# Kernel tuning notes

Hardware: AMD Instinct MI355X
Metric: run time of the kernel (lower is better)

Reference implementation:

```python
import jax, jax.numpy as jnp
import numpy as np

MARGIN = 1.0
EPS = 1e-6  # torch F.pairwise_distance default eps, added elementwise to (x - y)
NEG_INF = -1e30
POS_INF = 1e30


def _pairwise_dist_matrix(e):
    # D[i,j] = || e_i - e_j + EPS ||_2, expanded so we never materialize [B,B,D]:
    # ||d + eps||^2 = ||d||^2 + 2*eps*sum(d) + Dfeat*eps^2,  d = e_i - e_j
    sq = jnp.sum(e * e, axis=1)          # [B]
    s = jnp.sum(e, axis=1)               # [B]
    d2 = (sq[:, None] + sq[None, :] - 2.0 * (e @ e.T)
          + 2.0 * EPS * (s[:, None] - s[None, :])
          + e.shape[1] * (EPS * EPS))
    return jnp.sqrt(jnp.maximum(d2, 0.0))  # [B,B]


def _pdist(x, y):
    # F.pairwise_distance(p=2): ||x - y + eps||
    return jnp.sqrt(jnp.sum(jnp.square(x - y + EPS), axis=-1))


def setup_inputs() -> dict:
    B, D = 4096, 128
    key = jax.random.key(0)
    k1, k2, k3, k4 = jax.random.split(key, 4)
    embedding = jax.random.normal(k1, (B, D), dtype=jnp.float32)
    # label space == batch, each label appears exactly once in the batch
    target_idx = jax.random.permutation(k2, B).astype(jnp.int32)
    positive_idxs = jax.random.bernoulli(k3, 0.02, (B, B))  # [B, L] label-space mask
    negative_idxs = jax.random.bernoulli(k4, 0.5, (B, B))
    return {"embedding": embedding, "target_idx": target_idx,
            "positive_idxs": positive_idxs, "negative_idxs": negative_idxs}


def reference(embedding, target_idx, positive_idxs, negative_idxs):
    # Mining happens under no_grad in the original module.
    dm = jax.lax.stop_gradient(_pairwise_dist_matrix(embedding))  # [B,B]
    # batch j is a positive/negative candidate for anchor i iff its label is flagged
    pos_mask = positive_idxs[:, target_idx]  # [B,B] bool
    neg_mask = negative_idxs[:, target_idx]
    pos_idx = jnp.argmax(jnp.where(pos_mask, dm, NEG_INF), axis=1)  # hardest positive
    neg_idx = jnp.argmin(jnp.where(neg_mask, dm, POS_INF), axis=1)  # hardest negative
    valid = jnp.any(pos_mask, axis=1) & jnp.any(neg_mask, axis=1)
    a = embedding
    p = embedding[pos_idx]
    n = embedding[neg_idx]
    ap = _pdist(a, p)
    an = _pdist(a, n)
    pn = _pdist(p, n)
    loss = jax.nn.relu(ap - jnp.minimum(an, pn) + MARGIN)
    w = valid.astype(loss.dtype)
    return jnp.sum(loss * w) / jnp.maximum(jnp.sum(w), 1.0)
```

## Files before the change

### kernel.cpp

```cpp
#include <hip/hip_runtime.h>
#include <stdint.h>

#define BN 4096
#define DD 128
#define EPSF 1e-6f
#define MARGINF 1.0f
#define TM 128
#define TN 128
#define KC 64

typedef unsigned long long ull;
typedef short short8 __attribute__((ext_vector_type(8)));
typedef float f32x4 __attribute__((ext_vector_type(4)));

__device__ __forceinline__ unsigned int ord_f32(float f) {
    unsigned int u = __float_as_uint(f);
    return (u & 0x80000000u) ? ~u : (u | 0x80000000u);
}
__device__ __forceinline__ unsigned short bf16_rne(float x) {
    unsigned int u = __float_as_uint(x);
    return (unsigned short)((u + 0x7FFFu + ((u >> 16) & 1u)) >> 16);
}

__global__ void k_prep(const float* __restrict__ e, const int* __restrict__ tidx,
                       float* __restrict__ sq, float* __restrict__ s,
                       int* __restrict__ inv, ull* __restrict__ pk, ull* __restrict__ nk,
                       unsigned int* __restrict__ ehi, unsigned int* __restrict__ elo) {
    int w = threadIdx.x >> 6, lane = threadIdx.x & 63;
    int row = blockIdx.x * 4 + w;
    float2 v = ((const float2*)(e + (size_t)row * DD))[lane];
    unsigned short hx = bf16_rne(v.x), hy = bf16_rne(v.y);
    float rx = v.x - __uint_as_float((unsigned int)hx << 16);
    float ry = v.y - __uint_as_float((unsigned int)hy << 16);
    unsigned short lx = bf16_rne(rx), ly = bf16_rne(ry);
    ehi[row * 64 + lane] = (unsigned int)hx | ((unsigned int)hy << 16);
    elo[row * 64 + lane] = (unsigned int)lx | ((unsigned int)ly << 16);
    float ss = v.x + v.y;
    float qq = v.x * v.x + v.y * v.y;
    #pragma unroll
    for (int off = 32; off > 0; off >>= 1) {
        ss += __shfl_down(ss, off);
        qq += __shfl_down(qq, off);
    }
    if (lane == 0) {
        sq[row] = qq; s[row] = ss;
        inv[tidx[row]] = row;
        pk[row] = 0ULL; nk[row] = ~0ULL;
    }
}

__global__ void k_bits(const int* __restrict__ pos, const int* __restrict__ neg,
                       ull* __restrict__ pb, ull* __restrict__ nb) {
    int row = blockIdx.x;
    int w = threadIdx.x >> 6, lane = threadIdx.x & 63;
    const int* pr = pos + (size_t)row * BN;
    const int* nr = neg + (size_t)row * BN;
    #pragma unroll 4
    for (int g = 0; g < 16; g++) {
        int col = g * 256 + w * 64 + lane;
        ull b = __ballot(pr[col] != 0);
        if (lane == 0) pb[row * 64 + g * 4 + w] = b;
        b = __ballot(nr[col] != 0);
        if (lane == 0) nb[row * 64 + g * 4 + w] = b;
    }
}

__global__ __launch_bounds__(256, 2)
void k_select(const unsigned short* __restrict__ ehi, const unsigned short* __restrict__ elo,
              const float* __restrict__ sq, const float* __restrict__ s,
              const int* __restrict__ inv,
              const ull* __restrict__ pbits, const ull* __restrict__ nbits,
              ull* __restrict__ pkey, ull* __restrict__ nkey) {
    __shared__ __align__(16) char smem[73728];
    __shared__ int   jvs[TN];
    __shared__ float ri[TM], rj[TN];
    __shared__ ull   pbl[256], nbl[256];

    unsigned short* Ah = (unsigned short*)smem;
    unsigned short* Alo = Ah + 9216;
    unsigned short* Bh = Ah + 18432;
    unsigned short* Blo = Ah + 27648;
    float* Dl = (float*)smem;

    const int tid = threadIdx.x;
    const int i0 = blockIdx.x * TM;
    const int c0 = blockIdx.y * TN;

    if (tid < TN) {
        int j = inv[c0 + tid];
        jvs[tid] = j;
        rj[tid] = sq[j] - 2.0f * EPSF * s[j];
        ri[tid] = sq[i0 + tid] + 2.0f * EPSF * s[i0 + tid];
    }
    {
        int irow = tid >> 1, half = tid & 1;
        size_t bidx = (size_t)(i0 + irow) * 64 + (c0 >> 6) + half;
        pbl[tid] = pbits[bidx];
        nbl[tid] = nbits[bidx];
    }

    const int lane = tid & 63, w = tid >> 6;
    const int lrow = lane & 15, quad = lane >> 4;

    f32x4 acc[2][8];
    #pragma unroll
    for (int rt = 0; rt < 2; rt++)
        #pragma unroll
        for (int ct = 0; ct < 8; ct++)
            acc[rt][ct] = (f32x4){0.f, 0.f, 0.f, 0.f};

    for (int kc = 0; kc < DD / KC; kc++) {
        __syncthreads();
        {
            int rr0 = tid >> 3, seg = tid & 7;
            #pragma unroll
            for (int p = 0; p < 4; p++) {
                int rr = p * 32 + rr0;
                int ar = i0 + rr;
                int jr = jvs[rr];
                int4 va = ((const int4*)(ehi + (size_t)ar * DD))[kc * 8 + seg];
                int4 vb = ((const int4*)(elo + (size_t)ar * DD))[kc * 8 + seg];
                *(int4*)(Ah + rr * 72 + seg * 8) = va;
                *(int4*)(Alo + rr * 72 + seg * 8) = vb;
                va = ((const int4*)(ehi + (size_t)jr * DD))[kc * 8 + seg];
                vb = ((const int4*)(elo + (size_t)jr * DD))[kc * 8 + seg];
                *(int4*)(Bh + rr * 72 + seg * 8) = va;
                *(int4*)(Blo + rr * 72 + seg * 8) = vb;
            }
        }
        __syncthreads();

        #pragma unroll
        for (int ks = 0; ks < 2; ks++) {
            const int kof = ks * 32 + quad * 8;
            short8 ahi[2], alo2[2];
            #pragma unroll
            for (int rt = 0; rt < 2; rt++) {
                const unsigned short* ap = Ah + (w * 32 + rt * 16 + lrow) * 72 + kof;
                const unsigned short* lp = Alo + (w * 32 + rt * 16 + lrow) * 72 + kof;
                ahi[rt] = *(const short8*)ap;
                alo2[rt] = *(const short8*)lp;
            }
            #pragma unroll
            for (int ct = 0; ct < 8; ct++) {
                const unsigned short* bp = Bh + (ct * 16 + lrow) * 72 + kof;
                const unsigned short* blp = Blo + (ct * 16 + lrow) * 72 + kof;
                short8 bhi = *(const short8*)bp;
                short8 blo = *(const short8*)blp;
                #pragma unroll
                for (int rt = 0; rt < 2; rt++) {
                    acc[rt][ct] = __builtin_amdgcn_mfma_f32_16x16x32_bf16(ahi[rt], bhi, acc[rt][ct], 0, 0, 0);
                    acc[rt][ct] = __builtin_amdgcn_mfma_f32_16x16x32_bf16(ahi[rt], blo, acc[rt][ct], 0, 0, 0);
                    acc[rt][ct] = __builtin_amdgcn_mfma_f32_16x16x32_bf16(alo2[rt], bhi, acc[rt][ct], 0, 0, 0);
                }
            }
        }
    }

    __syncthreads();
    #pragma unroll
    for (int rt = 0; rt < 2; rt++)
        #pragma unroll
        for (int ct = 0; ct < 8; ct++) {
            int rbase = w * 32 + rt * 16 + quad * 4;
            int col = ct * 16 + lrow;
            #pragma unroll
            for (int t = 0; t < 4; t++)
                Dl[(rbase + t) * 132 + col] = acc[rt][ct][t];
        }
    __syncthreads();

    const int tx = tid & 15, ty = tid >> 4;
    float bpv[8], bnv[8]; int bpi[8], bni[8];
    #pragma unroll
    for (int r = 0; r < 8; r++) {
        bpv[r] = -3.4e38f; bnv[r] = 3.4e38f;
        bpi[r] = 0x7FFFFFFF; bni[r] = 0x7FFFFFFF;
    }
    const int shift = (tx & 7) * 8;
    #pragma unroll
    for (int r = 0; r < 8; r++) {
        int irow = ty * 8 + r;
        float4 d0 = *(const float4*)&Dl[irow * 132 + tx * 8];
        float4 d1 = *(const float4*)&Dl[irow * 132 + tx * 8 + 4];
        float dot[8] = {d0.x, d0.y, d0.z, d0.w, d1.x, d1.y, d1.z, d1.w};
        unsigned int pb = (unsigned int)((pbl[irow * 2 + (tx >> 3)] >> shift) & 0xFFu);
        unsigned int nb = (unsigned int)((nbl[irow * 2 + (tx >> 3)] >> shift) & 0xFFu);
        float riv = ri[irow];
        #pragma unroll
        for (int c = 0; c < 8; c++) {
            int jl = tx * 8 + c;
            float d2 = riv + rj[jl] - 2.0f * dot[c] + (float)DD * EPSF * EPSF;
            int j = jvs[jl];
            if ((pb >> c) & 1u) {
                if (d2 > bpv[r] || (d2 == bpv[r] && j < bpi[r])) { bpv[r] = d2; bpi[r] = j; }
            }
            if ((nb >> c) & 1u) {
                if (d2 < bnv[r] || (d2 == bnv[r] && j < bni[r])) { bnv[r] = d2; bni[r] = j; }
            }
        }
    }

    __syncthreads();
    float* spv = (float*)smem;
    int*   spi = (int*)(spv + 2048);
    float* snv = (float*)(spi + 2048);
    int*   sni = (int*)(snv + 2048);
    #pragma unroll
    for (int r = 0; r < 8; r++) {
        int row = ty * 8 + r;
        spv[row * 16 + tx] = bpv[r]; spi[row * 16 + tx] = bpi[r];
        snv[row * 16 + tx] = bnv[r]; sni[row * 16 + tx] = bni[r];
    }
    __syncthreads();
    if (tid < TM) {
        float bv = -3.4e38f, nv = 3.4e38f;
        int bi = 0x7FFFFFFF, ni = 0x7FFFFFFF;
        for (int t = 0; t < 16; t++) {
            float v = spv[tid * 16 + t]; int ix = spi[tid * 16 + t];
            if (ix != 0x7FFFFFFF && (v > bv || (v == bv && ix < bi))) { bv = v; bi = ix; }
            v = snv[tid * 16 + t]; ix = sni[tid * 16 + t];
            if (ix != 0x7FFFFFFF && (v < nv || (v == nv && ix < ni))) { nv = v; ni = ix; }
        }
        if (bi != 0x7FFFFFFF) {
            ull key = ((ull)ord_f32(bv) << 32) | (ull)(0xFFFFFFFFu - (unsigned)bi);
            atomicMax(&pkey[i0 + tid], key);
        }
        if (ni != 0x7FFFFFFF) {
            ull key = ((ull)ord_f32(nv) << 32) | (ull)(unsigned)ni;
            atomicMin(&nkey[i0 + tid], key);
        }
    }
}

__global__ void k_loss(const float* __restrict__ e,
                       const ull* __restrict__ pkey, const ull* __restrict__ nkey,
                       float* __restrict__ partials) {
    int w = threadIdx.x >> 6, lane = threadIdx.x & 63;
    int row = blockIdx.x * 4 + w;
    ull pk = pkey[row], nk = nkey[row];
    float loss = 0.0f, wt = 0.0f;
    if (pk != 0ULL && nk != ~0ULL) {
        int pi = (int)(0xFFFFFFFFu - (unsigned)(pk & 0xFFFFFFFFu));
        int ni = (int)(unsigned)(nk & 0xFFFFFFFFu);
        float2 av = ((const float2*)(e + (size_t)row * DD))[lane];
        float2 pv = ((const float2*)(e + (size_t)pi * DD))[lane];
        float2 nv = ((const float2*)(e + (size_t)ni * DD))[lane];
        float dx, dy;
        dx = av.x - pv.x + EPSF; dy = av.y - pv.y + EPSF;
        float ap2 = dx * dx + dy * dy;
        dx = av.x - nv.x + EPSF; dy = av.y - nv.y + EPSF;
        float an2 = dx * dx + dy * dy;
        dx = pv.x - nv.x + EPSF; dy = pv.y - nv.y + EPSF;
        float pn2 = dx * dx + dy * dy;
        #pragma unroll
        for (int off = 32; off > 0; off >>= 1) {
            ap2 += __shfl_down(ap2, off);
            an2 += __shfl_down(an2, off);
            pn2 += __shfl_down(pn2, off);
        }
        if (lane == 0) {
            float ap = sqrtf(ap2), an = sqrtf(an2), pn = sqrtf(pn2);
            loss = fmaxf(ap - fminf(an, pn) + MARGINF, 0.0f);
            wt = 1.0f;
        }
    }
    __shared__ float sl[4], sw[4];
    if (lane == 0) { sl[w] = loss; sw[w] = wt; }
    __syncthreads();
    if (threadIdx.x == 0) {
        partials[blockIdx.x * 2 + 0] = sl[0] + sl[1] + sl[2] + sl[3];
        partials[blockIdx.x * 2 + 1] = sw[0] + sw[1] + sw[2] + sw[3];
    }
}

__global__ void k_final(const float* __restrict__ partials, float* __restrict__ out) {
    int tid = threadIdx.x;
    float L = 0.0f, W = 0.0f;
    for (int i = 0; i < 4; i++) {
        int idx = tid + i * 256;
        L += partials[idx * 2];
        W += partials[idx * 2 + 1];
    }
    #pragma unroll
    for (int off = 32; off > 0; off >>= 1) {
        L += __shfl_down(L, off);
        W += __shfl_down(W, off);
    }
    __shared__ float sl[4], sw[4];
    int w = tid >> 6, lane = tid & 63;
    if (lane == 0) { sl[w] = L; sw[w] = W; }
    __syncthreads();
    if (tid == 0) {
        float Lt = sl[0] + sl[1] + sl[2] + sl[3];
        float Wt = sw[0] + sw[1] + sw[2] + sw[3];
        out[0] = Lt / fmaxf(Wt, 1.0f);
    }
}

extern "C" void kernel_launch(void* const* d_in, const int* in_sizes, int n_in,
                              void* d_out, int out_size, void* d_ws, size_t ws_size,
                              hipStream_t stream) {
    const float* e    = (const float*)d_in[0];
    const int*   tidx = (const int*)d_in[1];
    const int*   pos  = (const int*)d_in[2];
    const int*   neg  = (const int*)d_in[3];
    float* out = (float*)d_out;

    ull* pkey  = (ull*)d_ws;
    ull* nkey  = pkey + BN;
    ull* pbits = nkey + BN;
    ull* nbits = pbits + BN * 64;
    float* sq  = (float*)(nbits + BN * 64);
    float* s   = sq + BN;
    int* inv   = (int*)(s + BN);
    float* partials = (float*)(inv + BN);
    unsigned int* ehi = (unsigned int*)(partials + 2048);
    unsigned int* elo = ehi + BN * 64;

    k_prep<<<BN / 4, 256, 0, stream>>>(e, tidx, sq, s, inv, pkey, nkey, ehi, elo);
    k_bits<<<BN, 256, 0, stream>>>(pos, neg, pbits, nbits);
    dim3 grid(BN / TM, BN / TN);
    k_select<<<grid, 256, 0, stream>>>((const unsigned short*)ehi, (const unsigned short*)elo,
                                       sq, s, inv, pbits, nbits, pkey, nkey);
    k_loss<<<BN / 4, 256, 0, stream>>>(e, pkey, nkey, partials);
    k_final<<<1, 256, 0, stream>>>(partials, out);
}
```

Baseline: 209.2 us.

## Load MFMA operands directly from global, keep selection in registers, vectorize mask packing

The selection kernel stops staging the hi/lo bf16 operand tiles in shared memory. Each wave now loads its A and gathered B fragments straight from global memory into registers. Hardest positive and negative selection runs directly on the accumulator registers rather than going through a shared-memory distance tile, which removes several barriers and LDS round trips and allows three blocks per CU. The mask-packing kernel reads sixteen ints per thread with int4 loads and writes packed 16-bit words instead of using ballots. The cost is that the four waves each fetch the same B fragments, relying on L1/L2 to absorb the duplicated loads.

```diff
diff --git a/kernel.cpp b/kernel.cpp
--- a/kernel.cpp
+++ b/kernel.cpp
@@ -7,9 +7,9 @@
 #define MARGINF 1.0f
 #define TM 128
 #define TN 128
-#define KC 64
 
 typedef unsigned long long ull;
+typedef unsigned short ushort;
 typedef short short8 __attribute__((ext_vector_type(8)));
 typedef float f32x4 __attribute__((ext_vector_type(4)));
 
@@ -17,9 +17,9 @@
     unsigned int u = __float_as_uint(f);
     return (u & 0x80000000u) ? ~u : (u | 0x80000000u);
 }
-__device__ __forceinline__ unsigned short bf16_rne(float x) {
+__device__ __forceinline__ ushort bf16_rne(float x) {
     unsigned int u = __float_as_uint(x);
-    return (unsigned short)((u + 0x7FFFu + ((u >> 16) & 1u)) >> 16);
+    return (ushort)((u + 0x7FFFu + ((u >> 16) & 1u)) >> 16);
 }
 
 __global__ void k_prep(const float* __restrict__ e, const int* __restrict__ tidx,
@@ -29,10 +29,10 @@
     int w = threadIdx.x >> 6, lane = threadIdx.x & 63;
     int row = blockIdx.x * 4 + w;
     float2 v = ((const float2*)(e + (size_t)row * DD))[lane];
-    unsigned short hx = bf16_rne(v.x), hy = bf16_rne(v.y);
+    ushort hx = bf16_rne(v.x), hy = bf16_rne(v.y);
     float rx = v.x - __uint_as_float((unsigned int)hx << 16);
     float ry = v.y - __uint_as_float((unsigned int)hy << 16);
-    unsigned short lx = bf16_rne(rx), ly = bf16_rne(ry);
+    ushort lx = bf16_rne(rx), ly = bf16_rne(ry);
     ehi[row * 64 + lane] = (unsigned int)hx | ((unsigned int)hy << 16);
     elo[row * 64 + lane] = (unsigned int)lx | ((unsigned int)ly << 16);
     float ss = v.x + v.y;
@@ -50,57 +50,65 @@
 }
 
 __global__ void k_bits(const int* __restrict__ pos, const int* __restrict__ neg,
-                       ull* __restrict__ pb, ull* __restrict__ nb) {
-    int row = blockIdx.x;
-    int w = threadIdx.x >> 6, lane = threadIdx.x & 63;
-    const int* pr = pos + (size_t)row * BN;
-    const int* nr = neg + (size_t)row * BN;
-    #pragma unroll 4
-    for (int g = 0; g < 16; g++) {
-        int col = g * 256 + w * 64 + lane;
-        ull b = __ballot(pr[col] != 0);
-        if (lane == 0) pb[row * 64 + g * 4 + w] = b;
-        b = __ballot(nr[col] != 0);
-        if (lane == 0) nb[row * 64 + g * 4 + w] = b;
-    }
-}
-
-__global__ __launch_bounds__(256, 2)
-void k_select(const unsigned short* __restrict__ ehi, const unsigned short* __restrict__ elo,
+                       ushort* __restrict__ pb, ushort* __restrict__ nb) {
+    const int row = blockIdx.x, t = threadIdx.x;
+    const int4* pr = (const int4*)(pos + (size_t)row * BN) + t * 4;
+    const int4* nr = (const int4*)(neg + (size_t)row * BN) + t * 4;
+    int4 p0 = pr[0], p1 = pr[1], p2 = pr[2], p3 = pr[3];
+    int4 n0 = nr[0], n1 = nr[1], n2 = nr[2], n3 = nr[3];
+    unsigned int m = 0;
+    m |= (p0.x != 0) << 0;  m |= (p0.y != 0) << 1;  m |= (p0.z != 0) << 2;  m |= (p0.w != 0) << 3;
+    m |= (p1.x != 0) << 4;  m |= (p1.y != 0) << 5;  m |= (p1.z != 0) << 6;  m |= (p1.w != 0) << 7;
+    m |= (p2.x != 0) << 8;  m |= (p2.y != 0) << 9;  m |= (p2.z != 0) << 10; m |= (p2.w != 0) << 11;
+    m |= (p3.x != 0) << 12; m |= (p3.y != 0) << 13; m |= (p3.z != 0) << 14; m |= (p3.w != 0) << 15;
+    pb[(size_t)row * 256 + t] = (ushort)m;
+    m = 0;
+    m |= (n0.x != 0) << 0;  m |= (n0.y != 0) << 1;  m |= (n0.z != 0) << 2;  m |= (n0.w != 0) << 3;
+    m |= (n1.x != 0) << 4;  m |= (n1.y != 0) << 5;  m |= (n1.z != 0) << 6;  m |= (n1.w != 0) << 7;
+    m |= (n2.x != 0) << 8;  m |= (n2.y != 0) << 9;  m |= (n2.z != 0) << 10; m |= (n2.w != 0) << 11;
+    m |= (n3.x != 0) << 12; m |= (n3.y != 0) << 13; m |= (n3.z != 0) << 14; m |= (n3.w != 0) << 15;
+    nb[(size_t)row * 256 + t] = (ushort)m;
+}
+
+__global__ __launch_bounds__(256, 3)
+void k_select(const ushort* __restrict__ ehi, const ushort* __restrict__ elo,
               const float* __restrict__ sq, const float* __restrict__ s,
               const int* __restrict__ inv,
               const ull* __restrict__ pbits, const ull* __restrict__ nbits,
               ull* __restrict__ pkey, ull* __restrict__ nkey) {
-    __shared__ __align__(16) char smem[73728];
-    __shared__ int   jvs[TN];
-    __shared__ float ri[TM], rj[TN];
-    __shared__ ull   pbl[256], nbl[256];
-
-    unsigned short* Ah = (unsigned short*)smem;
-    unsigned short* Alo = Ah + 9216;
-    unsigned short* Bh = Ah + 18432;
-    unsigned short* Blo = Ah + 27648;
-    float* Dl = (float*)smem;
+    __shared__ float spv[2048]; __shared__ int spi[2048];
+    __shared__ float snv[2048]; __shared__ int sni[2048];
+    __shared__ ull pbl[256], nbl[256];
 
     const int tid = threadIdx.x;
-    const int i0 = blockIdx.x * TM;
-    const int c0 = blockIdx.y * TN;
-
-    if (tid < TN) {
-        int j = inv[c0 + tid];
-        jvs[tid] = j;
-        rj[tid] = sq[j] - 2.0f * EPSF * s[j];
-        ri[tid] = sq[i0 + tid] + 2.0f * EPSF * s[i0 + tid];
-    }
+    const int lane = tid & 63, w = tid >> 6;
+    const int lrow = lane & 15, quad = lane >> 4;
+    const int i0 = blockIdx.x * TM, c0 = blockIdx.y * TN;
+
     {
         int irow = tid >> 1, half = tid & 1;
-        size_t bidx = (size_t)(i0 + irow) * 64 + (c0 >> 6) + half;
-        pbl[tid] = pbits[bidx];
-        nbl[tid] = nbits[bidx];
-    }
-
-    const int lane = tid & 63, w = tid >> 6;
-    const int lrow = lane & 15, quad = lane >> 4;
+        size_t b = (size_t)(i0 + irow) * 64 + (c0 >> 6) + half;
+        pbl[tid] = pbits[b];
+        nbl[tid] = nbits[b];
+    }
+
+    int jreg[8]; float rjv[8];
+    #pragma unroll
+    for (int ct = 0; ct < 8; ct++) {
+        int j = inv[c0 + ct * 16 + lrow];
+        jreg[ct] = j;
+        rjv[ct] = sq[j] - 2.0f * EPSF * s[j];
+    }
+    float riv[8];
+    #pragma unroll
+    for (int rt = 0; rt < 2; rt++)
+        #pragma unroll
+        for (int t = 0; t < 4; t++) {
+            int row = i0 + w * 32 + rt * 16 + quad * 4 + t;
+            riv[rt * 4 + t] = sq[row] + 2.0f * EPSF * s[row];
+        }
+
+    __syncthreads();
 
     f32x4 acc[2][8];
     #pragma unroll
@@ -109,109 +117,70 @@
         for (int ct = 0; ct < 8; ct++)
             acc[rt][ct] = (f32x4){0.f, 0.f, 0.f, 0.f};
 
-    for (int kc = 0; kc < DD / KC; kc++) {
-        __syncthreads();
-        {
-            int rr0 = tid >> 3, seg = tid & 7;
-            #pragma unroll
-            for (int p = 0; p < 4; p++) {
-                int rr = p * 32 + rr0;
-                int ar = i0 + rr;
-                int jr = jvs[rr];
-                int4 va = ((const int4*)(ehi + (size_t)ar * DD))[kc * 8 + seg];
-                int4 vb = ((const int4*)(elo + (size_t)ar * DD))[kc * 8 + seg];
-                *(int4*)(Ah + rr * 72 + seg * 8) = va;
-                *(int4*)(Alo + rr * 72 + seg * 8) = vb;
-                va = ((const int4*)(ehi + (size_t)jr * DD))[kc * 8 + seg];
-                vb = ((const int4*)(elo + (size_t)jr * DD))[kc * 8 + seg];
-                *(int4*)(Bh + rr * 72 + seg * 8) = va;
-                *(int4*)(Blo + rr * 72 + seg * 8) = vb;
-            }
-        }
-        __syncthreads();
-
-        #pragma unroll
-        for (int ks = 0; ks < 2; ks++) {
-            const int kof = ks * 32 + quad * 8;
-            short8 ahi[2], alo2[2];
+    #pragma unroll
+    for (int kk = 0; kk < 4; kk++) {
+        const int kof = kk * 32 + quad * 8;
+        short8 ah[2], al[2];
+        #pragma unroll
+        for (int rt = 0; rt < 2; rt++) {
+            size_t off = (size_t)(i0 + w * 32 + rt * 16 + lrow) * DD + kof;
+            ah[rt] = *(const short8*)(ehi + off);
+            al[rt] = *(const short8*)(elo + off);
+        }
+        #pragma unroll
+        for (int ct = 0; ct < 8; ct++) {
+            size_t off = (size_t)jreg[ct] * DD + kof;
+            short8 bh = *(const short8*)(ehi + off);
+            short8 bl = *(const short8*)(elo + off);
             #pragma unroll
             for (int rt = 0; rt < 2; rt++) {
-                const unsigned short* ap = Ah + (w * 32 + rt * 16 + lrow) * 72 + kof;
-                const unsigned short* lp = Alo + (w * 32 + rt * 16 + lrow) * 72 + kof;
-                ahi[rt] = *(const short8*)ap;
-                alo2[rt] = *(const short8*)lp;
+                acc[rt][ct] = __builtin_amdgcn_mfma_f32_16x16x32_bf16(ah[rt], bh, acc[rt][ct], 0, 0, 0);
+                acc[rt][ct] = __builtin_amdgcn_mfma_f32_16x16x32_bf16(ah[rt], bl, acc[rt][ct], 0, 0, 0);
+                acc[rt][ct] = __builtin_amdgcn_mfma_f32_16x16x32_bf16(al[rt], bh, acc[rt][ct], 0, 0, 0);
             }
-            #pragma unroll
-            for (int ct = 0; ct < 8; ct++) {
-                const unsigned short* bp = Bh + (ct * 16 + lrow) * 72 + kof;
-                const unsigned short* blp = Blo + (ct * 16 + lrow) * 72 + kof;
-                short8 bhi = *(const short8*)bp;
-                short8 blo = *(const short8*)blp;
-                #pragma unroll
-                for (int rt = 0; rt < 2; rt++) {
-                    acc[rt][ct] = __builtin_amdgcn_mfma_f32_16x16x32_bf16(ahi[rt], bhi, acc[rt][ct], 0, 0, 0);
-                    acc[rt][ct] = __builtin_amdgcn_mfma_f32_16x16x32_bf16(ahi[rt], blo, acc[rt][ct], 0, 0, 0);
-                    acc[rt][ct] = __builtin_amdgcn_mfma_f32_16x16x32_bf16(alo2[rt], bhi, acc[rt][ct], 0, 0, 0);
-                }
-            }
-        }
-    }
-
-    __syncthreads();
-    #pragma unroll
-    for (int rt = 0; rt < 2; rt++)
-        #pragma unroll
-        for (int ct = 0; ct < 8; ct++) {
-            int rbase = w * 32 + rt * 16 + quad * 4;
-            int col = ct * 16 + lrow;
-            #pragma unroll
-            for (int t = 0; t < 4; t++)
-                Dl[(rbase + t) * 132 + col] = acc[rt][ct][t];
-        }
-    __syncthreads();
-
-    const int tx = tid & 15, ty = tid >> 4;
+        }
+    }
+
     float bpv[8], bnv[8]; int bpi[8], bni[8];
     #pragma unroll
     for (int r = 0; r < 8; r++) {
         bpv[r] = -3.4e38f; bnv[r] = 3.4e38f;
         bpi[r] = 0x7FFFFFFF; bni[r] = 0x7FFFFFFF;
     }
-    const int shift = (tx & 7) * 8;
-    #pragma unroll
-    for (int r = 0; r < 8; r++) {
-        int irow = ty * 8 + r;
-        float4 d0 = *(const float4*)&Dl[irow * 132 + tx * 8];
-        float4 d1 = *(const float4*)&Dl[irow * 132 + tx * 8 + 4];
-        float dot[8] = {d0.x, d0.y, d0.z, d0.w, d1.x, d1.y, d1.z, d1.w};
-        unsigned int pb = (unsigned int)((pbl[irow * 2 + (tx >> 3)] >> shift) & 0xFFu);
-        unsigned int nb = (unsigned int)((nbl[irow * 2 + (tx >> 3)] >> shift) & 0xFFu);
-        float riv = ri[irow];
-        #pragma unroll
-        for (int c = 0; c < 8; c++) {
-            int jl = tx * 8 + c;
-            float d2 = riv + rj[jl] - 2.0f * dot[c] + (float)DD * EPSF * EPSF;
-            int j = jvs[jl];
-            if ((pb >> c) & 1u) {
-                if (d2 > bpv[r] || (d2 == bpv[r] && j < bpi[r])) { bpv[r] = d2; bpi[r] = j; }
+    #pragma unroll
+    for (int rt = 0; rt < 2; rt++)
+        #pragma unroll
+        for (int t = 0; t < 4; t++) {
+            const int r = rt * 4 + t;
+            const int row = w * 32 + rt * 16 + quad * 4 + t;
+            ull p0 = pbl[row * 2] >> lrow, p1 = pbl[row * 2 + 1] >> lrow;
+            ull n0 = nbl[row * 2] >> lrow, n1 = nbl[row * 2 + 1] >> lrow;
+            float rv = riv[r];
+            #pragma unroll
+            for (int ct = 0; ct < 8; ct++) {
+                float d2 = rv + rjv[ct] - 2.0f * acc[rt][ct][t] + (float)DD * EPSF * EPSF;
+                int j = jreg[ct];
+                int sh = (ct & 3) * 16;
+                ull pw = (ct < 4) ? p0 : p1;
+                ull nw = (ct < 4) ? n0 : n1;
+                if ((pw >> sh) & 1ULL) {
+                    if (d2 > bpv[r] || (d2 == bpv[r] && j < bpi[r])) { bpv[r] = d2; bpi[r] = j; }
+                }
+                if ((nw >> sh) & 1ULL) {
+                    if (d2 < bnv[r] || (d2 == bnv[r] && j < bni[r])) { bnv[r] = d2; bni[r] = j; }
+                }
             }
-            if ((nb >> c) & 1u) {
-                if (d2 < bnv[r] || (d2 == bnv[r] && j < bni[r])) { bnv[r] = d2; bni[r] = j; }
-            }
-        }
-    }
-
-    __syncthreads();
-    float* spv = (float*)smem;
-    int*   spi = (int*)(spv + 2048);
-    float* snv = (float*)(spi + 2048);
-    int*   sni = (int*)(snv + 2048);
-    #pragma unroll
-    for (int r = 0; r < 8; r++) {
-        int row = ty * 8 + r;
-        spv[row * 16 + tx] = bpv[r]; spi[row * 16 + tx] = bpi[r];
-        snv[row * 16 + tx] = bnv[r]; sni[row * 16 + tx] = bni[r];
-    }
+        }
+
+    #pragma unroll
+    for (int rt = 0; rt < 2; rt++)
+        #pragma unroll
+        for (int t = 0; t < 4; t++) {
+            const int r = rt * 4 + t;
+            const int row = w * 32 + rt * 16 + quad * 4 + t;
+            spv[row * 16 + lrow] = bpv[r]; spi[row * 16 + lrow] = bpi[r];
+            snv[row * 16 + lrow] = bnv[r]; sni[row * 16 + lrow] = bni[r];
+        }
     __syncthreads();
     if (tid < TM) {
         float bv = -3.4e38f, nv = 3.4e38f;
@@ -319,9 +288,9 @@
     unsigned int* elo = ehi + BN * 64;
 
     k_prep<<<BN / 4, 256, 0, stream>>>(e, tidx, sq, s, inv, pkey, nkey, ehi, elo);
-    k_bits<<<BN, 256, 0, stream>>>(pos, neg, pbits, nbits);
+    k_bits<<<BN, 256, 0, stream>>>(pos, neg, (ushort*)pbits, (ushort*)nbits);
     dim3 grid(BN / TM, BN / TN);
-    k_select<<<grid, 256, 0, stream>>>((const unsigned short*)ehi, (const unsigned short*)elo,
+    k_select<<<grid, 256, 0, stream>>>((const ushort*)ehi, (const ushort*)elo,
                                        sq, s, inv, pbits, nbits, pkey, nkey);
     k_loss<<<BN / 4, 256, 0, stream>>>(e, pkey, nkey, partials);
     k_final<<<1, 256, 0, stream>>>(partials, out);
```

After: 248.1 us. +18.6%, slower.
